# Optimization experiments

Hardware: AMD Instinct MI355X
Metric: run time of the kernel (lower is better)

## Reference

```python
import jax, jax.numpy as jnp
import numpy as np

B, T, I, H = 64, 512, 1024, 1024

def setup_inputs() -> dict:
    key = jax.random.key(0)
    k1, k2, k3, k4, k5 = jax.random.split(key, 5)
    s_x = 1.0 / np.sqrt(I)
    s_h = 1.0 / np.sqrt(H)
    return {
        "x": jax.random.normal(k1, (B, T, I), dtype=jnp.float32),
        "Wx": jax.random.uniform(k2, (I, H), minval=-s_x, maxval=s_x, dtype=jnp.float32),
        "bx": jax.random.uniform(k3, (H,), minval=-s_x, maxval=s_x, dtype=jnp.float32),
        "Wh": jax.random.uniform(k4, (H, H), minval=-s_h, maxval=s_h, dtype=jnp.float32),
        "bh": jax.random.uniform(k5, (H,), minval=-s_h, maxval=s_h, dtype=jnp.float32),
    }

def reference(x, Wx, bx, Wh, bh):
    # Precompute input projections for all timesteps in one big GEMM: [B,T,H]
    xproj = jnp.einsum("bti,ih->bth", x, Wx) + bx + bh
    h0 = jnp.zeros((x.shape[0], Wh.shape[0]), dtype=x.dtype)

    def step(h, xp_t):
        h_new = jnp.tanh(xp_t + h @ Wh)
        return h_new, h_new

    # scan over time: xproj transposed to [T,B,H]
    h_last, outs = jax.lax.scan(step, h0, jnp.swapaxes(xproj, 0, 1))
    return jnp.swapaxes(outs, 0, 1), h_last
```

## Files before the change

### kernel.cpp

```cpp
#include <hip/hip_runtime.h>


#define Bdim 64
#define Tdim 512
#define Idim 1024
#define Hdim 1024
#define Mdim (Bdim * Tdim)

typedef __attribute__((ext_vector_type(8))) short bf16x8;
typedef __attribute__((ext_vector_type(4))) float f32x4;
typedef __attribute__((ext_vector_type(4))) unsigned int u32x4;

__device__ __forceinline__ float tanh_fast(float x) {
  float e = __expf(2.0f * x);
  return 1.0f - 2.0f / (e + 1.0f);
}
__device__ __forceinline__ unsigned int f2bf(float f) {
  unsigned int u = __float_as_uint(f);
  return (u + 0x7FFFu + ((u >> 16) & 1u)) >> 16;
}
__device__ __forceinline__ unsigned int pack2(float lo, float hi) {
  return f2bf(lo) | (f2bf(hi) << 16);
}

__global__ __launch_bounds__(256) void cvt_transpose(
    const float* __restrict__ src, unsigned short* __restrict__ dst) {
  __shared__ float t[32][33];
  const int bx = blockIdx.x * 32;
  const int by = blockIdx.y * 32;
  const int ty = threadIdx.x >> 3;
  const int tx = threadIdx.x & 7;
  float4 v = *(const float4*)&src[(size_t)(by + ty) * 1024 + bx + tx * 4];
  t[ty][tx * 4 + 0] = v.x; t[ty][tx * 4 + 1] = v.y;
  t[ty][tx * 4 + 2] = v.z; t[ty][tx * 4 + 3] = v.w;
  __syncthreads();
  ushort4 o;
  o.x = (unsigned short)f2bf(t[tx * 4 + 0][ty]);
  o.y = (unsigned short)f2bf(t[tx * 4 + 1][ty]);
  o.z = (unsigned short)f2bf(t[tx * 4 + 2][ty]);
  o.w = (unsigned short)f2bf(t[tx * 4 + 3][ty]);
  *(ushort4*)&dst[(size_t)(bx + ty) * 1024 + by + tx * 4] = o;
}

__global__ __launch_bounds__(256) void xg_mfma(
    const float* __restrict__ X,
    const unsigned short* __restrict__ WxT,
    const float* __restrict__ bx, const float* __restrict__ bh,
    float* __restrict__ C) {
  __shared__ char sAB[16384] __attribute__((aligned(16)));
  char* sA = sAB;
  char* sB = sAB + 8192;
  const int tid = threadIdx.x;
  const int m0 = blockIdx.y * 128;
  const int n0 = blockIdx.x * 128;
  const int w = tid >> 6, l = tid & 63;
  const int wm = (w >> 1) * 64, wn = (w & 1) * 64;
  const int r2 = tid >> 1, kh = tid & 1;

  f32x4 acc[4][4];
#pragma unroll
  for (int i = 0; i < 4; ++i)
#pragma unroll
    for (int j = 0; j < 4; ++j) acc[i][j] = (f32x4){0.f, 0.f, 0.f, 0.f};

  for (int k0 = 0; k0 < Idim; k0 += 32) {
    const float* xa = &X[(size_t)(m0 + r2) * Idim + k0 + kh * 16];
    float4 a0 = *(const float4*)(xa + 0), a1 = *(const float4*)(xa + 4);
    float4 a2 = *(const float4*)(xa + 8), a3 = *(const float4*)(xa + 12);
    const char* wb = (const char*)&WxT[(size_t)(n0 + r2) * Idim + k0 + kh * 16];
    u32x4 b0 = *(const u32x4*)wb;
    u32x4 b1 = *(const u32x4*)(wb + 16);
    __syncthreads();
    u32x4 pa0 = {pack2(a0.x, a0.y), pack2(a0.z, a0.w),
                 pack2(a1.x, a1.y), pack2(a1.z, a1.w)};
    u32x4 pa1 = {pack2(a2.x, a2.y), pack2(a2.z, a2.w),
                 pack2(a3.x, a3.y), pack2(a3.z, a3.w)};
    const int sw = (r2 & 7) << 4;
    const int rb = r2 * 64 + kh * 32;
    *(u32x4*)(sA + ((rb + 0) ^ sw)) = pa0;
    *(u32x4*)(sA + ((rb + 16) ^ sw)) = pa1;
    *(u32x4*)(sB + ((rb + 0) ^ sw)) = b0;
    *(u32x4*)(sB + ((rb + 16) ^ sw)) = b1;
    __syncthreads();
    bf16x8 af[4], bf[4];
#pragma unroll
    for (int i = 0; i < 4; ++i) {
      int ra = wm + i * 16 + (l & 15);
      af[i] = *(const bf16x8*)(sA + ((ra * 64 + (l >> 4) * 16) ^ ((ra & 7) << 4)));
      int rn = wn + i * 16 + (l & 15);
      bf[i] = *(const bf16x8*)(sB + ((rn * 64 + (l >> 4) * 16) ^ ((rn & 7) << 4)));
    }
#pragma unroll
    for (int i = 0; i < 4; ++i)
#pragma unroll
      for (int j = 0; j < 4; ++j)
        acc[i][j] = __builtin_amdgcn_mfma_f32_16x16x32_bf16(af[i], bf[j],
                                                            acc[i][j], 0, 0, 0);
  }
  float bias[4];
#pragma unroll
  for (int j = 0; j < 4; ++j) {
    int cc = n0 + wn + j * 16 + (l & 15);
    bias[j] = bx[cc] + bh[cc];
  }
#pragma unroll
  for (int i = 0; i < 4; ++i) {
    int rbase = m0 + wm + i * 16 + (l >> 4) * 4;
#pragma unroll
    for (int j = 0; j < 4; ++j) {
      int cc = n0 + wn + j * 16 + (l & 15);
#pragma unroll
      for (int r = 0; r < 4; ++r)
        C[(size_t)(rbase + r) * Hdim + cc] = acc[i][j][r] + bias[j];
    }
  }
}

__global__ void clear_flags(unsigned int* flags) {
  __hip_atomic_store(&flags[threadIdx.x], 0u, __ATOMIC_RELAXED,
                     __HIP_MEMORY_SCOPE_AGENT);
}

__global__ __launch_bounds__(512, 2) void rnn_scan(
    const unsigned short* __restrict__ WhT,
    float* __restrict__ out,
    float* __restrict__ hlast,
    unsigned int* hbuf,
    unsigned int* flags) {
  const int bid = blockIdx.x;
  const int c = bid & 7;
  const int m = bid >> 3;
  const int tid = threadIdx.x;
  const int w = tid >> 6;
  const int l = tid & 63;
  const int n0 = m * 128;

  __shared__ char smem[16384 + 66560] __attribute__((aligned(16)));
  char* smh = smem;
  char* smp = smem + 16384;

  bf16x8 bfrag[32];
  {
    const int kb = (w << 7) + ((l >> 4) << 3);
    const int col = n0 + (l & 15);
#pragma unroll
    for (int nt = 0; nt < 8; ++nt)
#pragma unroll
      for (int kt = 0; kt < 4; ++kt)
        bfrag[nt * 4 + kt] =
            *(const bf16x8*)&WhT[(size_t)(col + nt * 16) * 1024 + kb + kt * 32];
  }

  const int fb = tid >> 6;
  const int cpl = tid & 63;
  const int c0 = cpl * 2;
  const int b_abs = c * 8 + fb;
  const int nt0 = c0 >> 4;
  const int lane0 = ((fb >> 2) << 4) | (c0 & 15);
  const int regb = (fb & 3) * 4;
  const size_t obase = (size_t)b_abs * ((size_t)Tdim * Hdim) + n0 + c0;
  unsigned int* pub = &hbuf[(size_t)b_abs * 512 + m * 64 + cpl];
  unsigned int* myflag = &flags[c * 32 + m];
  const unsigned int* pollf = &flags[c * 32 + (l & 7)];

  float2 xp = *(const float2*)&out[obase];

  for (int t = 0; t < Tdim; ++t) {
    float sum0 = 0.f, sum1 = 0.f;
    if (t > 0) {
      const int arow = l & 7;
      const int abase = arow * 2048 + (w << 8) + ((l >> 4) << 4);
      const int sw = arow << 4;
      bf16x8 af[4];
#pragma unroll
      for (int kt = 0; kt < 4; ++kt)
        af[kt] = *(const bf16x8*)(smh + ((abase + kt * 64) ^ sw));
#pragma unroll
      for (int nt = 0; nt < 8; ++nt) {
        f32x4 a = {0.f, 0.f, 0.f, 0.f};
#pragma unroll
        for (int kt = 0; kt < 4; ++kt)
          a = __builtin_amdgcn_mfma_f32_16x16x32_bf16(af[kt], bfrag[nt * 4 + kt],
                                                      a, 0, 0, 0);
        *(f32x4*)(smp + (((w * 8 + nt) * 65 + l) << 4)) = a;
      }
      asm volatile("s_waitcnt lgkmcnt(0)" ::: "memory");
      __builtin_amdgcn_s_barrier();
      asm volatile("" ::: "memory");
#pragma unroll
      for (int w8 = 0; w8 < 8; ++w8) {
        const char* p = smp + (((w8 * 8 + nt0) * 65 + lane0) << 4) + regb;
        sum0 += *(const float*)p;
        sum1 += *(const float*)(p + 16);
      }
    }
    float h0 = tanh_fast(xp.x + sum0);
    float h1 = tanh_fast(xp.y + sum1);
    if (t == Tdim - 1) {
      *(float2*)&out[obase + (size_t)t * Hdim] = make_float2(h0, h1);
      *(float2*)&hlast[(size_t)b_abs * Hdim + n0 + c0] = make_float2(h0, h1);
      break;
    }
    const int par = (t + 1) & 1;
    __hip_atomic_store(pub + par * 32768, pack2(h0, h1), __ATOMIC_RELAXED,
                       __HIP_MEMORY_SCOPE_AGENT);
    asm volatile("" ::: "memory");
    *(float2*)&out[obase + (size_t)t * Hdim] = make_float2(h0, h1);
    xp = *(const float2*)&out[obase + (size_t)(t + 1) * Hdim];
    asm volatile("s_waitcnt vmcnt(2)" ::: "memory");
    __builtin_amdgcn_s_barrier();
    asm volatile("" ::: "memory");
    if (tid == 0)
      __hip_atomic_store(myflag, (unsigned int)(t + 1), __ATOMIC_RELAXED,
                         __HIP_MEMORY_SCOPE_AGENT);
    if (w == 7) {
      const unsigned int tgt = (unsigned int)(t + 1);
      for (;;) {
        unsigned int v;
        asm volatile(
            "global_load_dword %0, %1, off sc0 sc1\n\ts_waitcnt vmcnt(0)"
            : "=v"(v) : "v"(pollf) : "memory");
        if (__ballot(v >= tgt) == ~0ull) break;
        __builtin_amdgcn_s_sleep(2);
      }
    }
    asm volatile("" ::: "memory");
    __builtin_amdgcn_s_barrier();
    asm volatile("" ::: "memory");
    {
      const char* src = (const char*)hbuf + (size_t)par * 131072 +
                        (size_t)(c * 8 + (tid >> 6)) * 2048 + (tid & 63) * 32;
      u32x4 d0, d1;
      asm volatile(
          "global_load_dwordx4 %0, %2, off sc0 sc1\n\t"
          "global_load_dwordx4 %1, %2, off offset:16 sc0 sc1\n\t"
          "s_waitcnt vmcnt(0)"
          : "=&v"(d0), "=&v"(d1) : "v"(src) : "memory");
      __builtin_amdgcn_sched_barrier(0);
      const int r = tid >> 6;
      const int base = r * 2048 + (tid & 63) * 32;
      const int sw = r << 4;
      *(u32x4*)(smh + (base ^ sw)) = d0;
      *(u32x4*)(smh + ((base + 16) ^ sw)) = d1;
    }
    asm volatile("s_waitcnt lgkmcnt(0)" ::: "memory");
    __builtin_amdgcn_s_barrier();
    asm volatile("" ::: "memory");
  }
}

extern "C" void kernel_launch(void* const* d_in, const int* in_sizes, int n_in,
                              void* d_out, int out_size, void* d_ws,
                              size_t ws_size, hipStream_t stream) {
  const float* x  = (const float*)d_in[0];
  const float* Wx = (const float*)d_in[1];
  const float* bx = (const float*)d_in[2];
  const float* Wh = (const float*)d_in[3];
  const float* bh = (const float*)d_in[4];
  float* out = (float*)d_out;
  float* hlast = out + (size_t)Bdim * Tdim * Hdim;
  unsigned int* flags = (unsigned int*)d_ws;
  unsigned int* hbuf = (unsigned int*)((char*)d_ws + 4096);
  unsigned short* WxT = (unsigned short*)((char*)d_ws + 4096 + 262144);
  unsigned short* WhT = (unsigned short*)((char*)d_ws + 4096 + 262144 + 2097152);

  clear_flags<<<1, dim3(256), 0, stream>>>(flags);
  dim3 gt(32, 32);
  cvt_transpose<<<gt, dim3(256), 0, stream>>>(Wx, WxT);
  cvt_transpose<<<gt, dim3(256), 0, stream>>>(Wh, WhT);
  xg_mfma<<<dim3(Hdim / 128, Mdim / 128), dim3(256), 0, stream>>>(x, WxT, bx,
                                                                  bh, out);
  rnn_scan<<<dim3(64), dim3(512), 0, stream>>>(WhT, out, hlast, hbuf, flags);
}
```

Baseline: 1.546 ms.

## Replace block barriers with per-wave flags in recurrent scan and trim LDS partials

Each wave now publishes its own progress flag and spins on all 64 per-wave flags of its batch group. This removes the block-wide barriers and the single-thread flag publish from the serial per-timestep path. The poll loop no longer sleeps, and the output store plus next-xproj load move after the wait so they sit off the critical path. Only lanes holding the 8 valid MFMA rows write partial sums, which halves the LDS partial buffer. The cost is that every wave now polls, adding cache-coherent global traffic and spin pressure.

```diff
diff --git a/kernel.cpp b/kernel.cpp
--- a/kernel.cpp
+++ b/kernel.cpp
@@ -135,7 +135,7 @@
   const int l = tid & 63;
   const int n0 = m * 128;
 
-  __shared__ char smem[16384 + 66560] __attribute__((aligned(16)));
+  __shared__ char smem[16384 + 33792] __attribute__((aligned(16)));
   char* smh = smem;
   char* smp = smem + 16384;
 
@@ -151,17 +151,16 @@
             *(const bf16x8*)&WhT[(size_t)(col + nt * 16) * 1024 + kb + kt * 32];
   }
 
-  const int fb = tid >> 6;
-  const int cpl = tid & 63;
+  const int cpl = l;
   const int c0 = cpl * 2;
-  const int b_abs = c * 8 + fb;
+  const int b_abs = c * 8 + w;
   const int nt0 = c0 >> 4;
-  const int lane0 = ((fb >> 2) << 4) | (c0 & 15);
-  const int regb = (fb & 3) * 4;
+  const int lane0 = ((w >> 2) << 4) | (c0 & 15);
+  const int regb = (w & 3) * 4;
   const size_t obase = (size_t)b_abs * ((size_t)Tdim * Hdim) + n0 + c0;
   unsigned int* pub = &hbuf[(size_t)b_abs * 512 + m * 64 + cpl];
-  unsigned int* myflag = &flags[c * 32 + m];
-  const unsigned int* pollf = &flags[c * 32 + (l & 7)];
+  unsigned int* myflag = &flags[c * 64 + m * 8 + w];
+  const unsigned int* pollf = &flags[c * 64 + l];
 
   float2 xp = *(const float2*)&out[obase];
 
@@ -182,14 +181,15 @@
         for (int kt = 0; kt < 4; ++kt)
           a = __builtin_amdgcn_mfma_f32_16x16x32_bf16(af[kt], bfrag[nt * 4 + kt],
                                                       a, 0, 0, 0);
-        *(f32x4*)(smp + (((w * 8 + nt) * 65 + l) << 4)) = a;
+        if (l < 32)
+          *(f32x4*)(smp + (((w * 8 + nt) * 33 + l) << 4)) = a;
       }
       asm volatile("s_waitcnt lgkmcnt(0)" ::: "memory");
       __builtin_amdgcn_s_barrier();
       asm volatile("" ::: "memory");
 #pragma unroll
       for (int w8 = 0; w8 < 8; ++w8) {
-        const char* p = smp + (((w8 * 8 + nt0) * 65 + lane0) << 4) + regb;
+        const char* p = smp + (((w8 * 8 + nt0) * 33 + lane0) << 4) + regb;
         sum0 += *(const float*)p;
         sum1 += *(const float*)(p + 16);
       }
@@ -204,16 +204,11 @@
     const int par = (t + 1) & 1;
     __hip_atomic_store(pub + par * 32768, pack2(h0, h1), __ATOMIC_RELAXED,
                        __HIP_MEMORY_SCOPE_AGENT);
-    asm volatile("" ::: "memory");
-    *(float2*)&out[obase + (size_t)t * Hdim] = make_float2(h0, h1);
-    xp = *(const float2*)&out[obase + (size_t)(t + 1) * Hdim];
-    asm volatile("s_waitcnt vmcnt(2)" ::: "memory");
-    __builtin_amdgcn_s_barrier();
-    asm volatile("" ::: "memory");
-    if (tid == 0)
+    asm volatile("s_waitcnt vmcnt(0)" ::: "memory");
+    if (l == 0)
       __hip_atomic_store(myflag, (unsigned int)(t + 1), __ATOMIC_RELAXED,
                          __HIP_MEMORY_SCOPE_AGENT);
-    if (w == 7) {
+    {
       const unsigned int tgt = (unsigned int)(t + 1);
       for (;;) {
         unsigned int v;
@@ -221,15 +216,13 @@
             "global_load_dword %0, %1, off sc0 sc1\n\ts_waitcnt vmcnt(0)"
             : "=v"(v) : "v"(pollf) : "memory");
         if (__ballot(v >= tgt) == ~0ull) break;
-        __builtin_amdgcn_s_sleep(2);
       }
     }
-    asm volatile("" ::: "memory");
-    __builtin_amdgcn_s_barrier();
-    asm volatile("" ::: "memory");
+    *(float2*)&out[obase + (size_t)t * Hdim] = make_float2(h0, h1);
+    xp = *(const float2*)&out[obase + (size_t)(t + 1) * Hdim];
     {
       const char* src = (const char*)hbuf + (size_t)par * 131072 +
-                        (size_t)(c * 8 + (tid >> 6)) * 2048 + (tid & 63) * 32;
+                        (size_t)(c * 8 + w) * 2048 + l * 32;
       u32x4 d0, d1;
       asm volatile(
           "global_load_dwordx4 %0, %2, off sc0 sc1\n\t"
@@ -237,9 +230,8 @@
           "s_waitcnt vmcnt(0)"
           : "=&v"(d0), "=&v"(d1) : "v"(src) : "memory");
       __builtin_amdgcn_sched_barrier(0);
-      const int r = tid >> 6;
-      const int base = r * 2048 + (tid & 63) * 32;
-      const int sw = r << 4;
+      const int base = w * 2048 + l * 32;
+      const int sw = w << 4;
       *(u32x4*)(smh + (base ^ sw)) = d0;
       *(u32x4*)(smh + ((base + 16) ^ sw)) = d1;
     }
@@ -264,7 +256,7 @@
   unsigned short* WxT = (unsigned short*)((char*)d_ws + 4096 + 262144);
   unsigned short* WhT = (unsigned short*)((char*)d_ws + 4096 + 262144 + 2097152);
 
-  clear_flags<<<1, dim3(256), 0, stream>>>(flags);
+  clear_flags<<<1, dim3(512), 0, stream>>>(flags);
   dim3 gt(32, 32);
   cvt_transpose<<<gt, dim3(256), 0, stream>>>(Wx, WxT);
   cvt_transpose<<<gt, dim3(256), 0, stream>>>(Wh, WhT);
```

After: 4.362 ms. 2.82x slower.
